# Kernel tuning notes

Hardware: AMD Instinct MI355X
Metric: run time of the kernel (lower is better)

## Reference

```python
import jax, jax.numpy as jnp
import numpy as np

B, T, C, H = 4, 2048, 1024, 16
D = C // H  # head dim = 64


def setup_inputs() -> dict:
    key = jax.random.key(0)
    k_x, k_wa, k_ba, k_wp, k_bp = jax.random.split(key, 5)
    s = 1.0 / np.sqrt(C)
    return {
        "x": jax.random.normal(k_x, (B, T, C), dtype=jnp.float32),
        "w_attn": jax.random.uniform(k_wa, (C, 3 * C), minval=-s, maxval=s, dtype=jnp.float32),
        "b_attn": jax.random.uniform(k_ba, (3 * C,), minval=-s, maxval=s, dtype=jnp.float32),
        "w_proj": jax.random.uniform(k_wp, (C, C), minval=-s, maxval=s, dtype=jnp.float32),
        "b_proj": jax.random.uniform(k_bp, (C,), minval=-s, maxval=s, dtype=jnp.float32),
    }


def reference(x, w_attn, b_attn, w_proj, b_proj):
    b, t, c = x.shape
    qkv = x @ w_attn + b_attn  # [b, t, 3c]
    q, k, v = jnp.split(qkv, 3, axis=-1)
    # [b, h, t, d]
    q = q.reshape(b, t, H, D).transpose(0, 2, 1, 3)
    k = k.reshape(b, t, H, D).transpose(0, 2, 1, 3)
    v = v.reshape(b, t, H, D).transpose(0, 2, 1, 3)
    scale = 1.0 / np.sqrt(D)
    logits = jnp.einsum("bhqd,bhkd->bhqk", q, k) * scale
    causal = jnp.tril(jnp.ones((t, t), dtype=bool))
    logits = jnp.where(causal, logits, jnp.finfo(logits.dtype).min)
    attn = jax.nn.softmax(logits, axis=-1)
    y = jnp.einsum("bhqk,bhkd->bhqd", attn, v)
    y = y.transpose(0, 2, 1, 3).reshape(b, t, c)
    return y @ w_proj + b_proj
```

## Files before the change

kernel.cpp:

```cpp
#include <hip/hip_runtime.h>


using u16 = unsigned short;
using u32 = unsigned int;
using bf16x8 = __attribute__((ext_vector_type(8))) __bf16;
using f32x4  = __attribute__((ext_vector_type(4))) float;
using u16x8  = __attribute__((ext_vector_type(8))) u16;
using u16x4  = __attribute__((ext_vector_type(4))) u16;
using u32x2  = __attribute__((ext_vector_type(2))) u32;
using fvec4  = __attribute__((ext_vector_type(4))) float;

__device__ __forceinline__ u16 f2bf(float f) {
  u32 u = __builtin_bit_cast(u32, f);
  u32 r = (u + 0x7FFFu + ((u >> 16) & 1u)) >> 16;
  return (u16)r;
}

__device__ __forceinline__ u32 cvtpk(float lo, float hi) {
  u32 r;
  asm("v_cvt_pk_bf16_f32 %0, %1, %2" : "=v"(r) : "v"(lo), "v"(hi));
  return r;
}

__device__ __forceinline__ f32x4 mfma16(bf16x8 a, bf16x8 b, f32x4 c) {
  return __builtin_amdgcn_mfma_f32_16x16x32_bf16(a, b, c, 0, 0, 0);
}

__device__ __forceinline__ void gld16(const u16* g, u16* l) {
  __builtin_amdgcn_global_load_lds(
      (const __attribute__((address_space(1))) void*)g,
      (__attribute__((address_space(3))) void*)l, 16, 0, 0);
}

__device__ __forceinline__ void lgkm_barrier() {
  asm volatile("s_waitcnt lgkmcnt(0)" ::: "memory");
  __builtin_amdgcn_s_barrier();
  __builtin_amdgcn_sched_barrier(0);
}

__device__ __forceinline__ u16* swz(u16* base, int row, int colByte) {
  return (u16*)((char*)base + row * 128 + (colByte ^ ((row & 7) << 4)));
}
__device__ __forceinline__ const u16* swzc(const u16* base, int row, int colByte) {
  return (const u16*)((const char*)base + row * 128 + (colByte ^ ((row & 7) << 4)));
}

__global__ __launch_bounds__(256) void conv_kernel(
    const float* __restrict__ in, u16* __restrict__ out) {
  const size_t i = ((size_t)blockIdx.x * 256 + threadIdx.x) * 8;
  fvec4 a = *(const fvec4*)(in + i);
  fvec4 b = *(const fvec4*)(in + i + 4);
  u16x8 h;
#pragma unroll
  for (int j = 0; j < 4; ++j) { h[j] = f2bf(a[j]); h[4 + j] = f2bf(b[j]); }
  *(u16x8*)(out + i) = h;
}

__global__ __launch_bounds__(256) void transpose_conv_kernel(
    const float* __restrict__ W, u16* __restrict__ Wt, int K, int N) {
  __shared__ float tile[32][33];
  const int n0 = blockIdx.x * 32, k0 = blockIdx.y * 32;
  const int tx = threadIdx.x, ty = threadIdx.y;
#pragma unroll
  for (int j = 0; j < 4; ++j)
    tile[ty + j * 8][tx] = W[(size_t)(k0 + ty + j * 8) * N + n0 + tx];
  __syncthreads();
#pragma unroll
  for (int j = 0; j < 4; ++j)
    Wt[(size_t)(n0 + ty + j * 8) * K + k0 + tx] = f2bf(tile[tx][ty + j * 8]);
}

template <bool QKV>
__global__ __launch_bounds__(256) void gemm_kernel(
    const u16* __restrict__ A, const u16* __restrict__ Bt,
    const float* __restrict__ bias, void* __restrict__ Cp,
    u16* __restrict__ vt, int M, int N, int K) {
  constexpr float SC = 0.18033688011112042f;
  __shared__ u16 As[128 * 32];
  __shared__ u16 Bs[128 * 32];
  const int tid = threadIdx.x;
  const int lane = tid & 63;
  const int w = tid >> 6;
  const int wm = (w >> 1) * 64, wn = (w & 1) * 64;
  const int l15 = lane & 15, l16 = lane >> 4;

  const u32 nwg = gridDim.x * gridDim.y;
  u32 f = blockIdx.y * gridDim.x + blockIdx.x;
  f = (f & 7) * (nwg >> 3) + (f >> 3);
  const long mbase = (long)(f / gridDim.x) * 128;
  const long nbase = (long)(f % gridDim.x) * 128;

  const int srow = tid >> 2, scol = (tid & 3) * 8;
  const u16* ga = A + (mbase + srow) * (long)K + scol;
  const u16* gb = Bt + (nbase + srow) * (long)K + scol;
  u16* lA0 = &As[tid * 8];
  u16* lA1 = &As[2048 + tid * 8];
  u16* lB0 = &Bs[tid * 8];
  u16* lB1 = &Bs[2048 + tid * 8];

  f32x4 acc[4][4] = {};

  for (int kb = 0; kb < K; kb += 32) {
    __syncthreads();
    gld16(ga + kb, lA0);
    gld16(ga + 64 * (long)K + kb, lA1);
    gld16(gb + kb, lB0);
    gld16(gb + 64 * (long)K + kb, lB1);
    __syncthreads();

    bf16x8 af[4], bfr[4];
#pragma unroll
    for (int i = 0; i < 4; ++i) af[i] = *(const bf16x8*)(&As[(wm + i * 16 + l15) * 32 + l16 * 8]);
#pragma unroll
    for (int j = 0; j < 4; ++j) bfr[j] = *(const bf16x8*)(&Bs[(wn + j * 16 + l15) * 32 + l16 * 8]);
#pragma unroll
    for (int i = 0; i < 4; ++i)
#pragma unroll
      for (int j = 0; j < 4; ++j)
        acc[i][j] = mfma16(af[i], bfr[j], acc[i][j]);
  }

  if constexpr (QKV) {
    const bool isv = (nbase >= 2048);
#pragma unroll
    for (int i = 0; i < 4; ++i) {
#pragma unroll
      for (int j = 0; j < 4; ++j) {
        const long m0 = mbase + wm + i * 16 + l16 * 4;
        const int n = (int)nbase + wn + j * 16 + l15;
        const float bv = bias[n];
        if (!isv) {
          u16* qkp = (u16*)Cp;
          const float sc = (n < 1024) ? SC : 1.0f;
#pragma unroll
          for (int r = 0; r < 4; ++r)
            qkp[(m0 + r) * 2048 + n] = f2bf((acc[i][j][r] + bv) * sc);
        } else {
          const int vc = n - 2048, hh = vc >> 6, dd = vc & 63;
          const int bb = (int)(m0 >> 11), t0 = (int)(m0 & 2047);
          u16x4 pk;
#pragma unroll
          for (int r = 0; r < 4; ++r) pk[r] = f2bf(acc[i][j][r] + bv);
          *(u16x4*)(vt + ((size_t)(bb * 16 + hh) * 64 + dd) * 2048 + t0) = pk;
        }
      }
    }
  } else {
#pragma unroll
    for (int i = 0; i < 4; ++i) {
#pragma unroll
      for (int j = 0; j < 4; ++j) {
        const long row0 = mbase + wm + i * 16 + l16 * 4;
        const long col = nbase + wn + j * 16 + l15;
        const float bv = bias[col];
#pragma unroll
        for (int r = 0; r < 4; ++r)
          ((float*)Cp)[(row0 + r) * (long)N + col] = acc[i][j][r] + bv;
      }
    }
  }
}

__global__ __launch_bounds__(256, 2) void flash_kernel(
    const u16* __restrict__ qk, const u16* __restrict__ vt, u16* __restrict__ attn_out) {
  constexpr float MFIX = 4.0f;
  __shared__ u16 Ks[64 * 64];
  __shared__ u16 Vs[64 * 64];
  __shared__ u16 Ps[4 * 32 * 64];
  __shared__ float InvL[4][32];
  const int tid = threadIdx.x;
  const int lane = tid & 63, w = tid >> 6;
  const int l15 = lane & 15, l16 = lane >> 4;

  const u32 i = blockIdx.y * 8 + blockIdx.x;
  const int j = i >> 3;
  const int bh = (i & 7) | ((j & 7) << 3);
  const int pair = (int)(i >> 6);
  const int b = bh >> 4, h = bh & 15;
  const u16* qbase = qk + (size_t)b * 2048 * 2048 + h * 64;
  const u16* kbase = qbase + 1024;
  const u16* vbase = vt + (size_t)bh * 64 * 2048;
  u16* obase = attn_out + (size_t)b * 2048 * 1024 + h * 64;
  u16* PsW = Ps + w * 32 * 64;

  const int r0 = tid >> 3, c0 = (tid & 7) * 8;
  const int sco = ((c0 * 2) ^ ((r0 & 7) << 4)) >> 1;

  for (int half = 0; half < 2; ++half) {
    const int qt = half ? (15 - pair) : pair;
    const int nt = 2 * qt + 2;
    const int qr0 = qt * 128 + w * 32;

    bf16x8 qa[2][2];
#pragma unroll
    for (int fq = 0; fq < 2; ++fq)
#pragma unroll
      for (int ks = 0; ks < 2; ++ks)
        qa[fq][ks] = *(const bf16x8*)(qbase + (size_t)(qr0 + fq * 16 + l15) * 2048 + ks * 32 + l16 * 8);

    f32x4 o[2][4] = {};
    float lsum[2] = {0.f, 0.f};

    u16x8 kreg[2], vreg[2];
    kreg[0] = *(const u16x8*)(kbase + (size_t)r0 * 2048 + c0);
    kreg[1] = *(const u16x8*)(kbase + (size_t)(r0 + 32) * 2048 + c0);
    vreg[0] = *(const u16x8*)(vbase + (size_t)r0 * 2048 + c0);
    vreg[1] = *(const u16x8*)(vbase + (size_t)(r0 + 32) * 2048 + c0);

    for (int kt = 0; kt < nt; ++kt) {
      const int kb = kt * 64;
      lgkm_barrier();
      *(u16x8*)(&Ks[r0 * 64 + sco]) = kreg[0];
      *(u16x8*)(&Ks[(r0 + 32) * 64 + sco]) = kreg[1];
      *(u16x8*)(&Vs[r0 * 64 + sco]) = vreg[0];
      *(u16x8*)(&Vs[(r0 + 32) * 64 + sco]) = vreg[1];
      lgkm_barrier();
      if (kt + 1 < nt) {
        const int nb = kb + 64;
        kreg[0] = *(const u16x8*)(kbase + (size_t)(nb + r0) * 2048 + c0);
        kreg[1] = *(const u16x8*)(kbase + (size_t)(nb + r0 + 32) * 2048 + c0);
        vreg[0] = *(const u16x8*)(vbase + (size_t)r0 * 2048 + nb + c0);
        vreg[1] = *(const u16x8*)(vbase + (size_t)(r0 + 32) * 2048 + nb + c0);
      }

      f32x4 s[2][4];
      __builtin_amdgcn_s_setprio(1);
#pragma unroll
      for (int ni = 0; ni < 4; ++ni) {
        bf16x8 k0 = *(const bf16x8*)swzc(Ks, ni * 16 + l15, l16 * 16);
        bf16x8 k1 = *(const bf16x8*)swzc(Ks, ni * 16 + l15, 64 + l16 * 16);
        f32x4 t0 = {}, t1 = {};
        t0 = mfma16(k0, qa[0][0], t0);
        t0 = mfma16(k1, qa[0][1], t0);
        t1 = mfma16(k0, qa[1][0], t1);
        t1 = mfma16(k1, qa[1][1], t1);
        s[0][ni] = t0;
        s[1][ni] = t1;
      }
      __builtin_amdgcn_s_setprio(0);

      if (kb + 63 > qr0) {
#pragma unroll
        for (int fq = 0; fq < 2; ++fq) {
          const int qrow = qr0 + fq * 16 + l15;
#pragma unroll
          for (int ni = 0; ni < 4; ++ni)
#pragma unroll
            for (int r = 0; r < 4; ++r)
              if (kb + ni * 16 + l16 * 4 + r > qrow) s[fq][ni][r] = -1e30f;
        }
      }

#pragma unroll
      for (int fq = 0; fq < 2; ++fq) {
        float ps = 0.f;
        float p[4][4];
#pragma unroll
        for (int ni = 0; ni < 4; ++ni)
#pragma unroll
          for (int r = 0; r < 4; ++r) {
            p[ni][r] = exp2f(s[fq][ni][r] - MFIX);
            ps += p[ni][r];
          }
        lsum[fq] += ps;
#pragma unroll
        for (int ni = 0; ni < 4; ++ni) {
          u32x2 pk;
          pk[0] = cvtpk(p[ni][0], p[ni][1]);
          pk[1] = cvtpk(p[ni][2], p[ni][3]);
          *(u32x2*)swz(PsW, fq * 16 + l15, ni * 32 + l16 * 8) = pk;
        }
      }

      __builtin_amdgcn_s_setprio(1);
#pragma unroll
      for (int ki = 0; ki < 2; ++ki) {
        bf16x8 vb[4];
#pragma unroll
        for (int ni = 0; ni < 4; ++ni)
          vb[ni] = *(const bf16x8*)swzc(Vs, ni * 16 + l15, ki * 64 + l16 * 16);
#pragma unroll
        for (int fq = 0; fq < 2; ++fq) {
          bf16x8 pa = *(const bf16x8*)swzc(PsW, fq * 16 + l15, ki * 64 + l16 * 16);
#pragma unroll
          for (int ni = 0; ni < 4; ++ni)
            o[fq][ni] = mfma16(pa, vb[ni], o[fq][ni]);
        }
      }
      __builtin_amdgcn_s_setprio(0);
    }

#pragma unroll
    for (int fq = 0; fq < 2; ++fq) {
      float ls = lsum[fq];
      ls += __shfl_xor(ls, 16);
      ls += __shfl_xor(ls, 32);
      if (l16 == 0) InvL[w][fq * 16 + l15] = 1.0f / ls;
    }
    __builtin_amdgcn_wave_barrier();
#pragma unroll
    for (int fq = 0; fq < 2; ++fq) {
#pragma unroll
      for (int r = 0; r < 4; ++r) {
        const float ir = InvL[w][fq * 16 + l16 * 4 + r];
        const int t = qr0 + fq * 16 + l16 * 4 + r;
#pragma unroll
        for (int ni = 0; ni < 4; ++ni)
          obase[(size_t)t * 1024 + ni * 16 + l15] = f2bf(o[fq][ni][r] * ir);
      }
    }
  }
}

extern "C" void kernel_launch(void* const* d_in, const int* in_sizes, int n_in,
                              void* d_out, int out_size, void* d_ws, size_t ws_size,
                              hipStream_t stream) {
  (void)in_sizes; (void)n_in; (void)out_size; (void)ws_size;
  const float* x      = (const float*)d_in[0];
  const float* w_attn = (const float*)d_in[1];
  const float* b_attn = (const float*)d_in[2];
  const float* w_proj = (const float*)d_in[3];
  const float* b_proj = (const float*)d_in[4];
  float* out = (float*)d_out;

  char* ws = (char*)d_ws;
  u16* qkbuf = (u16*)(ws);
  u16* vtbuf = (u16*)(ws + 33554432);
  u16* xbf   = (u16*)(ws + 50331648);
  u16* attnb = (u16*)(ws + 50331648);
  u16* wtA   = (u16*)(ws + 67108864);
  u16* wtP   = (u16*)(ws + 73400320);

  conv_kernel<<<4096, 256, 0, stream>>>(x, xbf);
  transpose_conv_kernel<<<dim3(3072 / 32, 1024 / 32), dim3(32, 8), 0, stream>>>(w_attn, wtA, 1024, 3072);
  transpose_conv_kernel<<<dim3(1024 / 32, 1024 / 32), dim3(32, 8), 0, stream>>>(w_proj, wtP, 1024, 1024);

  gemm_kernel<true><<<dim3(3072 / 128, 8192 / 128), 256, 0, stream>>>(
      xbf, wtA, b_attn, qkbuf, vtbuf, 8192, 3072, 1024);

  flash_kernel<<<dim3(8, 64), 256, 0, stream>>>(qkbuf, vtbuf, attnb);

  gemm_kernel<false><<<dim3(1024 / 128, 8192 / 128), 256, 0, stream>>>(
      attnb, wtP, b_proj, out, nullptr, 8192, 1024, 1024);
}
```

Baseline: 188.8 us.

## Replace GEMMs with 256x256 tiled, double-buffered, swizzled 8-wave kernel

Both projection GEMMs move from a 128x128 tile with four waves and a single-buffered LDS stage to a 256x256 tile with eight waves. The new kernel uses double-buffered LDS fed by global_load_lds, an XOR swizzle against bank conflicts, and interleaved barriers so loads overlap MFMA clusters. The goal is more data reuse per loaded byte and hiding global latency. In exchange it needs 128 KB of LDS and more accumulator registers, and the grids shrink (384 and 128 blocks), which may underfill 256 CUs, especially for the output projection. The flash kernel's swizzle helpers are only inlined, with no behavioural change.

```diff
diff --git a/kernel.cpp b/kernel.cpp
--- a/kernel.cpp
+++ b/kernel.cpp
@@ -38,13 +38,6 @@
   __builtin_amdgcn_sched_barrier(0);
 }
 
-__device__ __forceinline__ u16* swz(u16* base, int row, int colByte) {
-  return (u16*)((char*)base + row * 128 + (colByte ^ ((row & 7) << 4)));
-}
-__device__ __forceinline__ const u16* swzc(const u16* base, int row, int colByte) {
-  return (const u16*)((const char*)base + row * 128 + (colByte ^ ((row & 7) << 4)));
-}
-
 __global__ __launch_bounds__(256) void conv_kernel(
     const float* __restrict__ in, u16* __restrict__ out) {
   const size_t i = ((size_t)blockIdx.x * 256 + threadIdx.x) * 8;
@@ -71,91 +64,166 @@
 }
 
 template <bool QKV>
-__global__ __launch_bounds__(256) void gemm_kernel(
+__global__ __launch_bounds__(512, 2) void gemm256_kernel(
     const u16* __restrict__ A, const u16* __restrict__ Bt,
     const float* __restrict__ bias, void* __restrict__ Cp,
     u16* __restrict__ vt, int M, int N, int K) {
   constexpr float SC = 0.18033688011112042f;
-  __shared__ u16 As[128 * 32];
-  __shared__ u16 Bs[128 * 32];
+  __shared__ u16 lds[2][4][8192];
   const int tid = threadIdx.x;
-  const int lane = tid & 63;
-  const int w = tid >> 6;
-  const int wm = (w >> 1) * 64, wn = (w & 1) * 64;
-  const int l15 = lane & 15, l16 = lane >> 4;
+  const int l = tid & 63, w = tid >> 6;
+  const int l15 = l & 15, l16 = l >> 4;
+  const int wr = w >> 2, wc = w & 3;
 
   const u32 nwg = gridDim.x * gridDim.y;
   u32 f = blockIdx.y * gridDim.x + blockIdx.x;
   f = (f & 7) * (nwg >> 3) + (f >> 3);
-  const long mbase = (long)(f / gridDim.x) * 128;
-  const long nbase = (long)(f % gridDim.x) * 128;
-
-  const int srow = tid >> 2, scol = (tid & 3) * 8;
-  const u16* ga = A + (mbase + srow) * (long)K + scol;
-  const u16* gb = Bt + (nbase + srow) * (long)K + scol;
-  u16* lA0 = &As[tid * 8];
-  u16* lA1 = &As[2048 + tid * 8];
-  u16* lB0 = &Bs[tid * 8];
-  u16* lB1 = &Bs[2048 + tid * 8];
-
-  f32x4 acc[4][4] = {};
-
-  for (int kb = 0; kb < K; kb += 32) {
-    __syncthreads();
-    gld16(ga + kb, lA0);
-    gld16(ga + 64 * (long)K + kb, lA1);
-    gld16(gb + kb, lB0);
-    gld16(gb + 64 * (long)K + kb, lB1);
-    __syncthreads();
-
-    bf16x8 af[4], bfr[4];
-#pragma unroll
-    for (int i = 0; i < 4; ++i) af[i] = *(const bf16x8*)(&As[(wm + i * 16 + l15) * 32 + l16 * 8]);
-#pragma unroll
-    for (int j = 0; j < 4; ++j) bfr[j] = *(const bf16x8*)(&Bs[(wn + j * 16 + l15) * 32 + l16 * 8]);
-#pragma unroll
-    for (int i = 0; i < 4; ++i)
-#pragma unroll
-      for (int j = 0; j < 4; ++j)
-        acc[i][j] = mfma16(af[i], bfr[j], acc[i][j]);
+  const int ntile = gridDim.x;
+  const long mbase = (long)(f / ntile) * 256;
+  const long nbase = (long)(f % ntile) * 256;
+
+  const int raS0 = w * 16 + (l >> 2);
+  const int raS1 = raS0 + 128;
+  const int scS0 = ((l & 3) ^ ((raS0 >> 1) & 3)) * 8;
+  const int scS1 = ((l & 3) ^ ((raS1 >> 1) & 3)) * 8;
+  const u16* gA0 = A + (mbase + raS0) * (long)K + scS0;
+  const u16* gA1 = A + (mbase + raS1) * (long)K + scS1;
+  const u16* gB0 = Bt + (nbase + raS0) * (long)K + scS0;
+  const u16* gB1 = Bt + (nbase + raS1) * (long)K + scS1;
+
+  const int raA = wr * 128 + l15;
+  const int offA = raA * 32 + ((l16 ^ ((raA >> 1) & 3)) * 8);
+  const int raB = wc * 64 + l15;
+  const int offB = raB * 32 + ((l16 ^ ((raB >> 1) & 3)) * 8);
+
+  f32x4 acc[8][4] = {};
+  bf16x8 af[4], bq[4];
+  const int NT = K >> 6;
+
+#define STAGE2(sb, reg, g0, g1, koff)               \
+  gld16((g0) + (koff), &lds[sb][reg][tid * 8]);     \
+  gld16((g1) + (koff), &lds[sb][reg][tid * 8 + 4096]);
+
+#define DSA(cb, mh, ks)                                                   \
+  { _Pragma("unroll") for (int i_ = 0; i_ < 4; ++i_)                      \
+      af[i_] = *(const bf16x8*)&lds[cb][ks][offA + ((mh)*4 + i_) * 512]; }
+
+#define DSB(cb, ks)                                                       \
+  { _Pragma("unroll") for (int j_ = 0; j_ < 4; ++j_)                      \
+      bq[j_] = *(const bf16x8*)&lds[cb][2 + (ks)][offB + j_ * 512]; }
+
+#define CLUSTER16(mh)                                                          \
+  __builtin_amdgcn_s_setprio(1);                                               \
+  _Pragma("unroll") for (int i_ = 0; i_ < 4; ++i_)                             \
+    _Pragma("unroll") for (int j_ = 0; j_ < 4; ++j_)                           \
+      acc[(mh)*4 + i_][j_] = mfma16(af[i_], bq[j_], acc[(mh)*4 + i_][j_]);     \
+  __builtin_amdgcn_s_setprio(0);
+
+#define BAR_LGKM()                                        \
+  __builtin_amdgcn_sched_barrier(0);                      \
+  __builtin_amdgcn_s_barrier();                           \
+  asm volatile("s_waitcnt lgkmcnt(0)" ::: "memory");      \
+  __builtin_amdgcn_sched_barrier(0)
+
+#define BAR_END()                     \
+  __builtin_amdgcn_sched_barrier(0);  \
+  __builtin_amdgcn_s_barrier()
+
+  STAGE2(0, 0, gA0, gA1, 0);
+  STAGE2(0, 2, gB0, gB1, 0);
+  STAGE2(0, 1, gA0, gA1, 32);
+  STAGE2(0, 3, gB0, gB1, 32);
+  asm volatile("s_waitcnt vmcnt(4)" ::: "memory");
+  __builtin_amdgcn_s_barrier();
+
+  for (int t = 0; t < NT - 1; ++t) {
+    const int cb = t & 1, sb = cb ^ 1;
+    const long kn = (long)(t + 1) * 64;
+    DSA(cb, 0, 0); DSB(cb, 0);
+    STAGE2(sb, 0, gA0, gA1, kn);
+    BAR_LGKM();
+    CLUSTER16(0);
+    BAR_END();
+    DSA(cb, 1, 0);
+    STAGE2(sb, 2, gB0, gB1, kn);
+    BAR_LGKM();
+    CLUSTER16(1);
+    asm volatile("s_waitcnt vmcnt(4)" ::: "memory");
+    BAR_END();
+    DSA(cb, 0, 1); DSB(cb, 1);
+    STAGE2(sb, 1, gA0, gA1, kn + 32);
+    BAR_LGKM();
+    CLUSTER16(0);
+    BAR_END();
+    DSA(cb, 1, 1);
+    STAGE2(sb, 3, gB0, gB1, kn + 32);
+    BAR_LGKM();
+    CLUSTER16(1);
+    asm volatile("s_waitcnt vmcnt(4)" ::: "memory");
+    BAR_END();
   }
+  {
+    const int cb = (NT - 1) & 1;
+    DSA(cb, 0, 0); DSB(cb, 0);
+    BAR_LGKM();
+    CLUSTER16(0);
+    BAR_END();
+    DSA(cb, 1, 0);
+    BAR_LGKM();
+    CLUSTER16(1);
+    asm volatile("s_waitcnt vmcnt(0)" ::: "memory");
+    BAR_END();
+    DSA(cb, 0, 1); DSB(cb, 1);
+    BAR_LGKM();
+    CLUSTER16(0);
+    BAR_END();
+    DSA(cb, 1, 1);
+    BAR_LGKM();
+    CLUSTER16(1);
+  }
+#undef STAGE2
+#undef DSA
+#undef DSB
+#undef CLUSTER16
+#undef BAR_LGKM
+#undef BAR_END
 
   if constexpr (QKV) {
     const bool isv = (nbase >= 2048);
 #pragma unroll
-    for (int i = 0; i < 4; ++i) {
-#pragma unroll
-      for (int j = 0; j < 4; ++j) {
-        const long m0 = mbase + wm + i * 16 + l16 * 4;
-        const int n = (int)nbase + wn + j * 16 + l15;
+    for (int mi = 0; mi < 8; ++mi) {
+#pragma unroll
+      for (int ni = 0; ni < 4; ++ni) {
+        const long m0 = mbase + wr * 128 + mi * 16 + l16 * 4;
+        const int n = (int)nbase + wc * 64 + ni * 16 + l15;
         const float bv = bias[n];
         if (!isv) {
           u16* qkp = (u16*)Cp;
           const float sc = (n < 1024) ? SC : 1.0f;
 #pragma unroll
           for (int r = 0; r < 4; ++r)
-            qkp[(m0 + r) * 2048 + n] = f2bf((acc[i][j][r] + bv) * sc);
+            qkp[(m0 + r) * 2048 + n] = f2bf((acc[mi][ni][r] + bv) * sc);
         } else {
           const int vc = n - 2048, hh = vc >> 6, dd = vc & 63;
           const int bb = (int)(m0 >> 11), t0 = (int)(m0 & 2047);
           u16x4 pk;
 #pragma unroll
-          for (int r = 0; r < 4; ++r) pk[r] = f2bf(acc[i][j][r] + bv);
+          for (int r = 0; r < 4; ++r) pk[r] = f2bf(acc[mi][ni][r] + bv);
           *(u16x4*)(vt + ((size_t)(bb * 16 + hh) * 64 + dd) * 2048 + t0) = pk;
         }
       }
     }
   } else {
 #pragma unroll
-    for (int i = 0; i < 4; ++i) {
-#pragma unroll
-      for (int j = 0; j < 4; ++j) {
-        const long row0 = mbase + wm + i * 16 + l16 * 4;
-        const long col = nbase + wn + j * 16 + l15;
+    for (int mi = 0; mi < 8; ++mi) {
+#pragma unroll
+      for (int ni = 0; ni < 4; ++ni) {
+        const long row0 = mbase + wr * 128 + mi * 16 + l16 * 4;
+        const long col = nbase + wc * 64 + ni * 16 + l15;
         const float bv = bias[col];
 #pragma unroll
         for (int r = 0; r < 4; ++r)
-          ((float*)Cp)[(row0 + r) * (long)N + col] = acc[i][j][r] + bv;
+          ((float*)Cp)[(row0 + r) * (long)N + col] = acc[mi][ni][r] + bv;
       }
     }
   }
@@ -227,8 +295,9 @@
       __builtin_amdgcn_s_setprio(1);
 #pragma unroll
       for (int ni = 0; ni < 4; ++ni) {
-        bf16x8 k0 = *(const bf16x8*)swzc(Ks, ni * 16 + l15, l16 * 16);
-        bf16x8 k1 = *(const bf16x8*)swzc(Ks, ni * 16 + l15, 64 + l16 * 16);
+        const int row = ni * 16 + l15;
+        bf16x8 k0 = *(const bf16x8*)((const char*)Ks + row * 128 + ((l16 * 16) ^ ((row & 7) << 4)));
+        bf16x8 k1 = *(const bf16x8*)((const char*)Ks + row * 128 + ((64 + l16 * 16) ^ ((row & 7) << 4)));
         f32x4 t0 = {}, t1 = {};
         t0 = mfma16(k0, qa[0][0], t0);
         t0 = mfma16(k1, qa[0][1], t0);
@@ -268,7 +337,8 @@
           u32x2 pk;
           pk[0] = cvtpk(p[ni][0], p[ni][1]);
           pk[1] = cvtpk(p[ni][2], p[ni][3]);
-          *(u32x2*)swz(PsW, fq * 16 + l15, ni * 32 + l16 * 8) = pk;
+          const int row = fq * 16 + l15;
+          *(u32x2*)((char*)PsW + row * 128 + ((ni * 32 + l16 * 8) ^ ((row & 7) << 4))) = pk;
         }
       }
 
@@ -277,11 +347,14 @@
       for (int ki = 0; ki < 2; ++ki) {
         bf16x8 vb[4];
 #pragma unroll
-        for (int ni = 0; ni < 4; ++ni)
-          vb[ni] = *(const bf16x8*)swzc(Vs, ni * 16 + l15, ki * 64 + l16 * 16);
+        for (int ni = 0; ni < 4; ++ni) {
+          const int row = ni * 16 + l15;
+          vb[ni] = *(const bf16x8*)((const char*)Vs + row * 128 + ((ki * 64 + l16 * 16) ^ ((row & 7) << 4)));
+        }
 #pragma unroll
         for (int fq = 0; fq < 2; ++fq) {
-          bf16x8 pa = *(const bf16x8*)swzc(PsW, fq * 16 + l15, ki * 64 + l16 * 16);
+          const int row = fq * 16 + l15;
+          bf16x8 pa = *(const bf16x8*)((const char*)PsW + row * 128 + ((ki * 64 + l16 * 16) ^ ((row & 7) << 4)));
 #pragma unroll
           for (int ni = 0; ni < 4; ++ni)
             o[fq][ni] = mfma16(pa, vb[ni], o[fq][ni]);
@@ -335,11 +408,11 @@
   transpose_conv_kernel<<<dim3(3072 / 32, 1024 / 32), dim3(32, 8), 0, stream>>>(w_attn, wtA, 1024, 3072);
   transpose_conv_kernel<<<dim3(1024 / 32, 1024 / 32), dim3(32, 8), 0, stream>>>(w_proj, wtP, 1024, 1024);
 
-  gemm_kernel<true><<<dim3(3072 / 128, 8192 / 128), 256, 0, stream>>>(
+  gemm256_kernel<true><<<dim3(3072 / 256, 8192 / 256), 512, 0, stream>>>(
       xbf, wtA, b_attn, qkbuf, vtbuf, 8192, 3072, 1024);
 
   flash_kernel<<<dim3(8, 64), 256, 0, stream>>>(qkbuf, vtbuf, attnb);
 
-  gemm_kernel<false><<<dim3(1024 / 128, 8192 / 128), 256, 0, stream>>>(
+  gemm256_kernel<false><<<dim3(1024 / 256, 8192 / 256), 512, 0, stream>>>(
       attnb, wtP, b_proj, out, nullptr, 8192, 1024, 1024);
 }
```

Measured after the change: 185.8 us. About the same (-1.6%).
